# Optimization experiments

Measured on AMD Instinct MI355X. Metric: run time of the kernel, lower is better.

The kernel has to match this reference:

```python
import jax, jax.numpy as jnp
import numpy as np

B, L, HE, HD, E, AP, T = 128, 128, 1024, 1024, 512, 512, 64

def _lstm_cell(x, h, c, W_ih, W_hh, b_ih, b_hh):
    # torch LSTMCell: gates ordered i, f, g, o
    g = x @ W_ih + b_ih + h @ W_hh + b_hh
    i, f, gg, o = jnp.split(g, 4, axis=-1)
    c_new = jax.nn.sigmoid(f) * c + jax.nn.sigmoid(i) * jnp.tanh(gg)
    h_new = jax.nn.sigmoid(o) * jnp.tanh(c_new)
    return h_new, c_new

def setup_inputs() -> dict:
    key = jax.random.key(0)
    ks = jax.random.split(key, 24)
    def rn(k, shape, scale=0.02):
        return jax.random.normal(k, shape, dtype=jnp.float32) * scale
    inp = {
        "enc_hiddens": jax.random.normal(ks[0], (B, L, HE), dtype=jnp.float32),
        "enc_masks": jnp.zeros((B, L), dtype=jnp.int32),
        "h1_0": rn(ks[1], (B, HD), 1.0), "c1_0": rn(ks[2], (B, HD), 1.0),
        "h2_0": rn(ks[3], (B, HD), 1.0), "c2_0": rn(ks[4], (B, HD), 1.0),
        "captions": jax.random.normal(ks[5], (T, B, E), dtype=jnp.float32),
        # attention params
        "att_W": rn(ks[6], (HE, AP)), "att_b": jnp.zeros((AP,), jnp.float32),
        "dhp_W": rn(ks[7], (HD, AP)), "dhp_b": jnp.zeros((AP,), jnp.float32),
        "corr_w": rn(ks[8], (AP,)), "corr_b": jnp.zeros((), jnp.float32),
        "lt_W": rn(ks[9], (HD, HD)), "lt_b": jnp.zeros((HD,), jnp.float32),
        # LSTM cell 1: input E + HE
        "W_ih1": rn(ks[10], (E + HE, 4 * HD)), "W_hh1": rn(ks[11], (HD, 4 * HD)),
        "b_ih1": jnp.zeros((4 * HD,), jnp.float32), "b_hh1": jnp.zeros((4 * HD,), jnp.float32),
        # LSTM cell 2: input HD
        "W_ih2": rn(ks[12], (HD, 4 * HD)), "W_hh2": rn(ks[13], (HD, 4 * HD)),
        "b_ih2": jnp.zeros((4 * HD,), jnp.float32), "b_hh2": jnp.zeros((4 * HD,), jnp.float32),
    }
    return inp

def reference(enc_hiddens, enc_masks, h1_0, c1_0, h2_0, c2_0, captions,
              att_W, att_b, dhp_W, dhp_b, corr_w, corr_b, lt_W, lt_b,
              W_ih1, W_hh1, b_ih1, b_hh1, W_ih2, W_hh2, b_ih2, b_hh2):
    mask = enc_masks.astype(bool)                      # True == masked (pad)
    enc_proj = enc_hiddens @ att_W + att_b             # (B, L, AP)
    h_prev0 = jnp.ones((enc_hiddens.shape[0], HD), dtype=enc_hiddens.dtype) / HE

    def step(carry, x_t):
        h_prev, h1, c1, h2, c2 = carry
        q = h_prev @ dhp_W + dhp_b                     # (B, AP)
        e = jnp.tanh(enc_proj + q[:, None, :]) @ corr_w + corr_b  # (B, L)
        e = jnp.where(mask, -jnp.inf, e)
        alpha = jax.nn.softmax(e, axis=1)
        a_t = jnp.einsum('bl,blh->bh', alpha, enc_hiddens)
        lstm_in = jnp.concatenate([x_t, a_t], axis=1)
        h1n, c1n = _lstm_cell(lstm_in, h1, c1, W_ih1, W_hh1, b_ih1, b_hh1)
        h2n, c2n = _lstm_cell(h1n, h2, c2, W_ih2, W_hh2, b_ih2, b_hh2)
        # note: output uses layer-1 hidden (matches original); dropout is eval/no-op
        out_t = jnp.tanh(h1n @ lt_W + lt_b)
        # num_decoder_layers == 2 -> next h_prev is layer-2 hidden
        return (h2n, h1n, c1n, h2n, c2n), out_t

    _, outputs = jax.lax.scan(step, (h_prev0, h1_0, c1_0, h2_0, c2_0), captions)
    return outputs                                      # (T, B, HD)
```

## Files before the change

kernel.cpp:

```cpp
#include <hip/hip_runtime.h>
#include <cstdint>
#include <cstddef>

#define DEVI __device__ __forceinline__

typedef __attribute__((ext_vector_type(8))) short short8;
typedef __attribute__((ext_vector_type(4))) float floatx4;
typedef __attribute__((ext_vector_type(4))) unsigned short ushortx4;

DEVI float bf2f(unsigned short u) { union { unsigned int i; float f; } v; v.i = ((unsigned int)u) << 16; return v.f; }
DEVI unsigned short f2bf(float f) {
  union { float f; unsigned int i; } v; v.f = f;
  unsigned int r = v.i + 0x7fffu + ((v.i >> 16) & 1u);
  return (unsigned short)(r >> 16);
}
DEVI float fsig(float x) { return 1.f / (1.f + __expf(-x)); }
DEVI float ftanh(float x) { return 1.f - 2.f / (__expf(2.f * x) + 1.f); }

DEVI unsigned ld32s(const unsigned* p) { return __hip_atomic_load(p, __ATOMIC_RELAXED, __HIP_MEMORY_SCOPE_AGENT); }
DEVI void st32s(unsigned* p, unsigned v) { __hip_atomic_store(p, v, __ATOMIC_RELAXED, __HIP_MEMORY_SCOPE_AGENT); }
DEVI unsigned add32s(unsigned* p, unsigned v) { return __hip_atomic_fetch_add(p, v, __ATOMIC_RELAXED, __HIP_MEMORY_SCOPE_AGENT); }

DEVI void bar_nd() { asm volatile("s_waitcnt lgkmcnt(0)\ns_barrier" ::: "memory"); }

struct PP {
  const float *c1_0, *c2_0;
  const float *att_b, *dhp_b, *corr_w, *corr_b, *lt_b;
  const float *b_ih1, *b_hh1, *b_ih2, *b_hh2;
  const int* masks;
  float* out;
  unsigned int* SY; float* q0acc;
  const unsigned short* ench; unsigned short* proj; const unsigned short* caps;
  const unsigned short *W1t, *W2t, *dhpWt, *ltWt, *attWt;
  unsigned short* at; unsigned short* h1b; unsigned short* h2b; float* q;
  float *c1ws, *c2ws;
};

DEVI void zero_g(float* g) {
  for (int i = threadIdx.x; i < 128 * 17; i += 1024) g[i] = 0.f;
}

DEVI int swzb(int row, int kb) { return row * 256 + (kb ^ ((row & 7) << 4)); }

template <int NC, typename AL>
DEVI void gemm_lds(float* g, unsigned short (*As)[16384], unsigned short (*Bs)[2048],
                   const unsigned short* Wtile, int ldw, AL al) {
  const int tid = threadIdx.x, wave = tid >> 6, lane = tid & 63;
  const int sr = tid >> 4, sk8 = (tid & 15) << 3;
  const int wA0 = swzb(sr, (tid & 15) << 4);
  const int wA1 = swzb(sr + 64, (tid & 15) << 4);
  const int wB = swzb(sr & 15, (tid & 15) << 4);
  const unsigned short* wrow = Wtile + (size_t)sr * ldw;
  const int m = wave & 7, kh = wave >> 3;
  const int arow = (m << 4) + (lane & 15);
  const int kq = (lane >> 4) << 3;
  const int rA0 = swzb(arow, (kh * 64 + kq) << 1);
  const int rA1 = swzb(arow, (kh * 64 + 32 + kq) << 1);
  const int rB0 = swzb(lane & 15, (kh * 64 + kq) << 1);
  const int rB1 = swzb(lane & 15, (kh * 64 + 32 + kq) << 1);

  short8 aA[2], aB[2], bA, bB;
  floatx4 acc = (floatx4){0.f, 0.f, 0.f, 0.f};

#define LDCHUNK(c, ra, rb)                                        \
  do {                                                            \
    ra[0] = *(const short8*)al(sr, (c)*128 + sk8);                \
    ra[1] = *(const short8*)al(sr + 64, (c)*128 + sk8);           \
    if (tid < 256) rb = *(const short8*)(wrow + (c)*128 + sk8);   \
  } while (0)
#define STCHUNK(b, ra, rb)                                        \
  do {                                                            \
    char* ab_ = (char*)As[b];                                     \
    *(short8*)(ab_ + wA0) = ra[0];                                \
    *(short8*)(ab_ + wA1) = ra[1];                                \
    if (tid < 256) *(short8*)((char*)Bs[b] + wB) = rb;            \
  } while (0)
#define COMPCH(b)                                                 \
  do {                                                            \
    char* ab_ = (char*)As[b];                                     \
    char* bb_ = (char*)Bs[b];                                     \
    short8 x0 = *(const short8*)(ab_ + rA0);                      \
    short8 y0 = *(const short8*)(bb_ + rB0);                      \
    short8 x1 = *(const short8*)(ab_ + rA1);                      \
    short8 y1 = *(const short8*)(bb_ + rB1);                      \
    acc = __builtin_amdgcn_mfma_f32_16x16x32_bf16(x0, y0, acc, 0, 0, 0); \
    acc = __builtin_amdgcn_mfma_f32_16x16x32_bf16(x1, y1, acc, 0, 0, 0); \
  } while (0)

  LDCHUNK(0, aA, bA);
  LDCHUNK(1, aB, bB);
  STCHUNK(0, aA, bA);
  bar_nd();
#pragma unroll
  for (int c = 0; c < NC; c += 2) {
    if (c + 2 < NC) LDCHUNK(c + 2, aA, bA);
    COMPCH(0);
    STCHUNK(1, aB, bB);
    bar_nd();
    if (c + 3 < NC) LDCHUNK(c + 3, aB, bB);
    COMPCH(1);
    if (c + 2 < NC) STCHUNK(0, aA, bA);
    bar_nd();
  }
#undef LDCHUNK
#undef STCHUNK
#undef COMPCH

  const int col = lane & 15, rr = (lane >> 4) << 2;
#pragma unroll
  for (int r = 0; r < 4; ++r)
    atomicAdd(&g[((m << 4) + rr + r) * 17 + col], acc[r]);
}

DEVI int qidx(int a) { return a + (a >> 6); }

__global__ __launch_bounds__(1024, 4) void k1_attn(PP p, int t) {
  __shared__ float g[128 * 17];
  __shared__ unsigned short As[2][16384];
  __shared__ unsigned short Bs[2][2048];
  __shared__ float q_ss[520], corr_ss[520];
  __shared__ float alpha_s[128], e_s[128];
  __shared__ float redv[2];
  const int tid = threadIdx.x, blk = blockIdx.x;
  const int wave = tid >> 6, lane = tid & 63;

  if (blk < 32) {
    if (t >= 1 && t < 64) {
      zero_g(g);
      const unsigned short* h2p = p.h2b + ((((unsigned)t + 1u) & 1u) << 17);
      auto al = [&](int row, int k) -> const unsigned short* {
        return h2p + ((size_t)row << 10) + k;
      };
      gemm_lds<8>(g, As, Bs, p.dhpWt + (size_t)blk * 16 * 1024, 1024, al);
      __syncthreads();
      for (int e = tid; e < 2048; e += 1024) {
        const int b = e >> 4, col = e & 15, n = blk * 16 + col;
        const float qv = g[b * 17 + col] + p.dhp_b[n];
        st32s((unsigned*)(p.q + b * 512 + n), __float_as_uint(qv));
      }
      __builtin_amdgcn_s_waitcnt(0);
    }
    __syncthreads();
    if (tid == 0) add32s(&p.SY[4], 1u);
  } else if (blk < 160) {
    if (t < 64) {
      const int b = blk - 32;
      if (t >= 1) {
        if (tid == 0) {
          while (ld32s(&p.SY[4]) < (unsigned)(32 * (t + 1))) __builtin_amdgcn_s_sleep(1);
        }
        __syncthreads();
        if (tid < 512) q_ss[qidx(tid)] = __uint_as_float(ld32s((const unsigned*)(p.q + b * 512 + tid)));
      } else {
        if (tid < 512) q_ss[qidx(tid)] = p.q[b * 512 + tid];
      }
      if (tid < 512) corr_ss[qidx(tid)] = p.corr_w[tid];
      __syncthreads();
      {
        const int l = tid >> 3, l8 = tid & 7;
        const unsigned short* pp_ = p.proj + ((size_t)(b * 128 + l)) * 512 + l8 * 64;
        short8 vv[8];
#pragma unroll
        for (int j = 0; j < 8; ++j) vv[j] = *(const short8*)(pp_ + j * 8);
        float acc = 0.f;
#pragma unroll
        for (int j = 0; j < 8; ++j)
#pragma unroll
          for (int i = 0; i < 8; ++i) {
            const int ap = l8 * 64 + j * 8 + i;
            acc += ftanh(bf2f((unsigned short)vv[j][i]) + q_ss[qidx(ap)]) * corr_ss[qidx(ap)];
          }
        acc += __shfl_down(acc, 4, 8);
        acc += __shfl_down(acc, 2, 8);
        acc += __shfl_down(acc, 1, 8);
        if (l8 == 0) {
          acc += p.corr_b[0];
          if (p.masks[b * 128 + l] != 0) acc = -1e30f;
          e_s[l] = acc;
        }
      }
      __syncthreads();
      if (wave == 0) {
        float m0 = fmaxf(e_s[lane], e_s[lane + 64]);
#pragma unroll
        for (int off = 32; off; off >>= 1) m0 = fmaxf(m0, __shfl_xor(m0, off));
        const float a0 = __expf(e_s[lane] - m0), a1 = __expf(e_s[lane + 64] - m0);
        alpha_s[lane] = a0; alpha_s[lane + 64] = a1;
        float s = a0 + a1;
#pragma unroll
        for (int off = 32; off; off >>= 1) s += __shfl_xor(s, off);
        if (lane == 0) redv[0] = 1.f / s;
      }
      __syncthreads();
      {
        const float inv = redv[0];
        const unsigned short* pe = p.ench + ((size_t)b << 17) + tid;
        float acc = 0.f;
#pragma unroll 16
        for (int l = 0; l < 128; ++l) acc += alpha_s[l] * bf2f(pe[(size_t)l << 10]);
        p.at[(b << 10) + tid] = f2bf(acc * inv);
      }
    }
  } else {
    if (t >= 1) {
      const int ob = blk - 160, ot = t - 1;
      zero_g(g);
      const unsigned short* h1 = p.h1b + (((unsigned)ot & 1u) << 17);
      auto al = [&](int row, int k) -> const unsigned short* {
        return h1 + ((size_t)row << 10) + k;
      };
      gemm_lds<8>(g, As, Bs, p.ltWt + (size_t)ob * 16 * 1024, 1024, al);
      __syncthreads();
      for (int e = tid; e < 2048; e += 1024) {
        const int b = e >> 4, col = e & 15, n = ob * 16 + col;
        p.out[(size_t)ot * 131072 + (b << 10) + n] = ftanh(g[b * 17 + col] + p.lt_b[n]);
      }
    }
  }
}

__global__ __launch_bounds__(1024, 4) void k2_g1(PP p, int t) {
  __shared__ float g[128 * 17];
  __shared__ unsigned short As[2][16384];
  __shared__ unsigned short Bs[2][2048];
  const int tid = threadIdx.x, blk = blockIdx.x;
  zero_g(g);
  const unsigned short* caps_t = p.caps + ((size_t)t << 16);
  const unsigned short* h1p = p.h1b + ((((unsigned)t + 1u) & 1u) << 17);
  const unsigned short* at_ = p.at;
  auto al = [&](int row, int k) -> const unsigned short* {
    if (k < 512) return caps_t + ((size_t)row << 9) + k;
    if (k < 1536) return at_ + ((size_t)row << 10) + (k - 512);
    return h1p + ((size_t)row << 10) + (k - 1536);
  };
  gemm_lds<20>(g, As, Bs, p.W1t + (size_t)blk * 16 * 2560, 2560, al);
  __syncthreads();
  if (tid < 512) {
    const int b = tid >> 2, c = tid & 3;
    const int cidx = b * 1024 + blk * 4 + c;
    const float cprev = (t == 0) ? p.c1_0[cidx] : p.c1ws[cidx];
    const float gi = g[b * 17 + c]      + p.b_ih1[blk * 4 + c]        + p.b_hh1[blk * 4 + c];
    const float gf = g[b * 17 + 4 + c]  + p.b_ih1[1024 + blk * 4 + c] + p.b_hh1[1024 + blk * 4 + c];
    const float gg = g[b * 17 + 8 + c]  + p.b_ih1[2048 + blk * 4 + c] + p.b_hh1[2048 + blk * 4 + c];
    const float go = g[b * 17 + 12 + c] + p.b_ih1[3072 + blk * 4 + c] + p.b_hh1[3072 + blk * 4 + c];
    const float cn = fsig(gf) * cprev + fsig(gi) * ftanh(gg);
    p.c1ws[cidx] = cn;
    p.h1b[(((unsigned)t & 1u) << 17) + (b << 10) + blk * 4 + c] = f2bf(fsig(go) * ftanh(cn));
  }
}

__global__ __launch_bounds__(1024, 4) void k3_g2(PP p, int t) {
  __shared__ float g[128 * 17];
  __shared__ unsigned short As[2][16384];
  __shared__ unsigned short Bs[2][2048];
  const int tid = threadIdx.x, blk = blockIdx.x;
  zero_g(g);
  const unsigned short* h1c = p.h1b + (((unsigned)t & 1u) << 17);
  const unsigned short* h2p = p.h2b + ((((unsigned)t + 1u) & 1u) << 17);
  auto al = [&](int row, int k) -> const unsigned short* {
    if (k < 1024) return h1c + ((size_t)row << 10) + k;
    return h2p + ((size_t)row << 10) + (k - 1024);
  };
  gemm_lds<16>(g, As, Bs, p.W2t + (size_t)blk * 16 * 2048, 2048, al);
  __syncthreads();
  if (tid < 512) {
    const int b = tid >> 2, c = tid & 3;
    const int cidx = b * 1024 + blk * 4 + c;
    const float cprev = (t == 0) ? p.c2_0[cidx] : p.c2ws[cidx];
    const float gi = g[b * 17 + c]      + p.b_ih2[blk * 4 + c]        + p.b_hh2[blk * 4 + c];
    const float gf = g[b * 17 + 4 + c]  + p.b_ih2[1024 + blk * 4 + c] + p.b_hh2[1024 + blk * 4 + c];
    const float gg = g[b * 17 + 8 + c]  + p.b_ih2[2048 + blk * 4 + c] + p.b_hh2[2048 + blk * 4 + c];
    const float go = g[b * 17 + 12 + c] + p.b_ih2[3072 + blk * 4 + c] + p.b_hh2[3072 + blk * 4 + c];
    const float cn = fsig(gf) * cprev + fsig(gi) * ftanh(gg);
    p.c2ws[cidx] = cn;
    p.h2b[(((unsigned)t & 1u) << 17) + (b << 10) + blk * 4 + c] = f2bf(fsig(go) * ftanh(cn));
  }
}

__global__ __launch_bounds__(512) void k_zero(unsigned int* SY, float* q0) {
  SY[threadIdx.x] = 0u;
  q0[threadIdx.x] = 0.f;
}

__global__ __launch_bounds__(256) void k_cvt4(const float* caps, const float* ench,
                                              const float* h1_0, const float* h2_0,
                                              unsigned short* o_caps, unsigned short* o_ench,
                                              unsigned short* o_h1, unsigned short* o_h2) {
  const size_t i = ((size_t)blockIdx.x * 256 + threadIdx.x) << 2;
  const float* s; unsigned short* d; size_t off;
  if (i < 4194304u) { s = caps; d = o_caps; off = i; }
  else if (i < 20971520u) { s = ench; d = o_ench; off = i - 4194304u; }
  else if (i < 21102592u) { s = h1_0; d = o_h1; off = i - 20971520u; }
  else { s = h2_0; d = o_h2; off = i - 21102592u; }
  floatx4 v = *(const floatx4*)(s + off);
  ushortx4 o = { f2bf(v[0]), f2bf(v[1]), f2bf(v[2]), f2bf(v[3]) };
  *(ushortx4*)(d + off) = o;
}

__global__ __launch_bounds__(256) void k_tr(const float* srcA, const float* srcB, int ksplit,
                                            int K, int stride, int Nrows, int perm,
                                            unsigned short* out, float* q0) {
  __shared__ float lds[64][5];
  const int nbr = Nrows >> 2;
  const int rt = blockIdx.x % nbr, kt = blockIdx.x / nbr;
  const int r0 = rt * 4, k0 = kt * 64;
  int oc0;
  if (perm) { const int nb = r0 >> 4, gg = (r0 & 15) >> 2; oc0 = gg * 1024 + nb * 4; }
  else oc0 = r0;
  {
    const int kk = threadIdx.x >> 2, rr = threadIdx.x & 3;
    const int k = k0 + kk;
    const float* s = (k < ksplit) ? (srcA + (size_t)k * stride) : (srcB + (size_t)(k - ksplit) * stride);
    lds[kk][rr] = s[oc0 + rr];
  }
  __syncthreads();
  if (q0 != nullptr && threadIdx.x < 4) {
    float t = 0.f;
    for (int kk = 0; kk < 64; ++kk) t += lds[kk][threadIdx.x];
    atomicAdd(&q0[oc0 + threadIdx.x], t);
  }
  {
    const int rr = threadIdx.x >> 6, kk = threadIdx.x & 63;
    out[(size_t)(r0 + rr) * K + k0 + kk] = f2bf(lds[kk][rr]);
  }
}

__global__ __launch_bounds__(1024, 4) void k_proj2(PP p) {
  __shared__ unsigned short As[2][16384];
  __shared__ unsigned short Bs[2][16384];
  const int tid = threadIdx.x, blk = blockIdx.x;
  const int mb = blk >> 2, nb = blk & 3;
  const int m0 = mb << 7, n0 = nb << 7;
  const int wave = tid >> 6, lane = tid & 63;
  const int sr = tid >> 4, sk8 = (tid & 15) << 3;
  const int wL0 = swzb(sr, (tid & 15) << 4);
  const int wL1 = swzb(sr + 64, (tid & 15) << 4);
  const int mw = wave & 7, nh = wave >> 3;
  const int m16 = lane & 15, kq = (lane >> 4) << 3;
  const unsigned short* Ag  = p.ench  + ((size_t)(m0 + sr) << 10);
  const unsigned short* Ag2 = p.ench  + ((size_t)(m0 + sr + 64) << 10);
  const unsigned short* Bg  = p.attWt + ((size_t)(n0 + sr) << 10);
  const unsigned short* Bg2 = p.attWt + ((size_t)(n0 + sr + 64) << 10);

  const int ar = mw * 16 + m16;
  const int aBase = ar * 256, aX = (ar & 7) << 4;
  const int bX = (m16 & 7) << 4;
  int bBase[4];
#pragma unroll
  for (int nf = 0; nf < 4; ++nf) bBase[nf] = (nh * 64 + nf * 16 + m16) * 256;

  floatx4 acc[4];
#pragma unroll
  for (int nf = 0; nf < 4; ++nf) acc[nf] = (floatx4){0.f, 0.f, 0.f, 0.f};

  short8 xa0, xa1, xb0, xb1, ya0, ya1, yb0, yb1;

#define PJLD(c, r0_, r1_, r2_, r3_)                      \
  do {                                                   \
    r0_ = *(const short8*)(Ag + (c) * 128 + sk8);        \
    r1_ = *(const short8*)(Ag2 + (c) * 128 + sk8);       \
    r2_ = *(const short8*)(Bg + (c) * 128 + sk8);        \
    r3_ = *(const short8*)(Bg2 + (c) * 128 + sk8);       \
  } while (0)
#define PJST(b, r0_, r1_, r2_, r3_)                      \
  do {                                                   \
    *(short8*)((char*)As[b] + wL0) = r0_;                \
    *(short8*)((char*)As[b] + wL1) = r1_;                \
    *(short8*)((char*)Bs[b] + wL0) = r2_;                \
    *(short8*)((char*)Bs[b] + wL1) = r3_;                \
  } while (0)
#define PJCOMP(b)                                                        \
  do {                                                                   \
    char* ab_ = (char*)As[b];                                            \
    char* bb_ = (char*)Bs[b];                                            \
    _Pragma("unroll")                                                    \
    for (int ks = 0; ks < 4; ++ks) {                                     \
      const int kb = ks * 64 + (kq << 1);                                \
      short8 af = *(const short8*)(ab_ + aBase + (kb ^ aX));             \
      _Pragma("unroll")                                                  \
      for (int nf = 0; nf < 4; ++nf) {                                   \
        short8 bf = *(const short8*)(bb_ + bBase[nf] + (kb ^ bX));       \
        acc[nf] = __builtin_amdgcn_mfma_f32_16x16x32_bf16(af, bf, acc[nf], 0, 0, 0); \
      }                                                                  \
    }                                                                    \
  } while (0)

  PJLD(0, xa0, xa1, xb0, xb1);
  PJLD(1, ya0, ya1, yb0, yb1);
  PJST(0, xa0, xa1, xb0, xb1);
  bar_nd();
#pragma unroll
  for (int c = 0; c < 8; c += 2) {
    if (c + 2 < 8) PJLD(c + 2, xa0, xa1, xb0, xb1);
    PJCOMP(0);
    PJST(1, ya0, ya1, yb0, yb1);
    bar_nd();
    if (c + 3 < 8) PJLD(c + 3, ya0, ya1, yb0, yb1);
    PJCOMP(1);
    if (c + 2 < 8) PJST(0, xa0, xa1, xb0, xb1);
    bar_nd();
  }
#undef PJLD
#undef PJST
#undef PJCOMP

  const int r0 = (lane >> 4) << 2;
#pragma unroll
  for (int nf = 0; nf < 4; ++nf) {
    const int col = n0 + nh * 64 + nf * 16 + m16;
    const float ab = p.att_b[col];
#pragma unroll
    for (int r = 0; r < 4; ++r) {
      const int row = m0 + mw * 16 + r0 + r;
      p.proj[(size_t)row * 512 + col] = f2bf(acc[nf][r] + ab);
    }
  }
}

__global__ __launch_bounds__(1024) void k_qinit(float* q, const float* q0acc, const float* dhp_b) {
  const int i = blockIdx.x * 1024 + threadIdx.x;
  const int n = i & 511;
  q[i] = q0acc[n] * (1.f / 1024.f) + dhp_b[n];
}

extern "C" void kernel_launch(void* const* d_in, const int* in_sizes, int n_in,
                              void* d_out, int out_size, void* d_ws, size_t ws_size,
                              hipStream_t stream) {
  const float* enc_hiddens = (const float*)d_in[0];
  const int*   enc_masks   = (const int*)d_in[1];
  const float* h1_0 = (const float*)d_in[2];
  const float* c1_0 = (const float*)d_in[3];
  const float* h2_0 = (const float*)d_in[4];
  const float* c2_0 = (const float*)d_in[5];
  const float* captions = (const float*)d_in[6];
  const float* att_W = (const float*)d_in[7];
  const float* att_b = (const float*)d_in[8];
  const float* dhp_W = (const float*)d_in[9];
  const float* dhp_b = (const float*)d_in[10];
  const float* corr_w = (const float*)d_in[11];
  const float* corr_b = (const float*)d_in[12];
  const float* lt_W = (const float*)d_in[13];
  const float* lt_b = (const float*)d_in[14];
  const float* W_ih1 = (const float*)d_in[15];
  const float* W_hh1 = (const float*)d_in[16];
  const float* b_ih1 = (const float*)d_in[17];
  const float* b_hh1 = (const float*)d_in[18];
  const float* W_ih2 = (const float*)d_in[19];
  const float* W_hh2 = (const float*)d_in[20];
  const float* b_ih2 = (const float*)d_in[21];
  const float* b_hh2 = (const float*)d_in[22];

  uint8_t* w = (uint8_t*)d_ws;
  unsigned int* SY = (unsigned int*)w;
  float* q0acc = (float*)(w + 2048);
  size_t off = 4096;
  unsigned short* ench  = (unsigned short*)(w + off); off += 33554432;
  unsigned short* proj  = (unsigned short*)(w + off); off += 16777216;
  unsigned short* caps  = (unsigned short*)(w + off); off += 8388608;
  unsigned short* W1t   = (unsigned short*)(w + off); off += 20971520;
  unsigned short* W2t   = (unsigned short*)(w + off); off += 16777216;
  unsigned short* dhpWt = (unsigned short*)(w + off); off += 1048576;
  unsigned short* ltWt  = (unsigned short*)(w + off); off += 2097152;
  unsigned short* attWt = (unsigned short*)(w + off); off += 1048576;
  unsigned short* at_   = (unsigned short*)(w + off); off += 262144;
  unsigned short* h1b   = (unsigned short*)(w + off); off += 524288;
  unsigned short* h2b   = (unsigned short*)(w + off); off += 524288;
  float* qb             = (float*)(w + off);          off += 262144;
  float* c1ws           = (float*)(w + off);          off += 524288;
  float* c2ws           = (float*)(w + off);          off += 524288;
  if (ws_size < off) return;

  k_zero<<<1, 512, 0, stream>>>(SY, q0acc);
  k_cvt4<<<20736, 256, 0, stream>>>(captions, enc_hiddens, h1_0, h2_0,
                                    caps, ench, h1b + 131072, h2b + 131072);
  k_tr<<<40960, 256, 0, stream>>>(W_ih1, W_hh1, 1536, 2560, 4096, 4096, 1, W1t, nullptr);
  k_tr<<<32768, 256, 0, stream>>>(W_ih2, W_hh2, 1024, 2048, 4096, 4096, 1, W2t, nullptr);
  k_tr<<<2048, 256, 0, stream>>>(dhp_W, dhp_W, 1024, 1024, 512, 512, 0, dhpWt, q0acc);
  k_tr<<<4096, 256, 0, stream>>>(lt_W, lt_W, 1024, 1024, 1024, 1024, 0, ltWt, nullptr);
  k_tr<<<2048, 256, 0, stream>>>(att_W, att_W, 1024, 1024, 512, 512, 0, attWt, nullptr);
  k_qinit<<<64, 1024, 0, stream>>>(qb, q0acc, dhp_b);

  PP p;
  p.c1_0 = c1_0; p.c2_0 = c2_0;
  p.att_b = att_b; p.dhp_b = dhp_b; p.corr_w = corr_w; p.corr_b = corr_b; p.lt_b = lt_b;
  p.b_ih1 = b_ih1; p.b_hh1 = b_hh1; p.b_ih2 = b_ih2; p.b_hh2 = b_hh2;
  p.masks = enc_masks;
  p.out = (float*)d_out;
  p.SY = SY; p.q0acc = q0acc;
  p.ench = ench; p.proj = proj; p.caps = caps;
  p.W1t = W1t; p.W2t = W2t; p.dhpWt = dhpWt; p.ltWt = ltWt; p.attWt = attWt;
  p.at = at_; p.h1b = h1b; p.h2b = h2b; p.q = qb;
  p.c1ws = c1ws; p.c2ws = c2ws;

  k_proj2<<<512, 1024, 0, stream>>>(p);

  for (int t = 0; t < 64; ++t) {
    k1_attn<<<224, 1024, 0, stream>>>(p, t);
    k2_g1<<<256, 1024, 0, stream>>>(p, t);
    k3_g2<<<256, 1024, 0, stream>>>(p, t);
  }
  k1_attn<<<224, 1024, 0, stream>>>(p, 64);
}
```

Measured before the change: 4.831 ms.

## Fuse per-step kernels into one persistent kernel with global flag barriers

```diff
diff --git a/kernel.cpp b/kernel.cpp
--- a/kernel.cpp
+++ b/kernel.cpp
@@ -19,7 +19,18 @@
 
 DEVI unsigned ld32s(const unsigned* p) { return __hip_atomic_load(p, __ATOMIC_RELAXED, __HIP_MEMORY_SCOPE_AGENT); }
 DEVI void st32s(unsigned* p, unsigned v) { __hip_atomic_store(p, v, __ATOMIC_RELAXED, __HIP_MEMORY_SCOPE_AGENT); }
-DEVI unsigned add32s(unsigned* p, unsigned v) { return __hip_atomic_fetch_add(p, v, __ATOMIC_RELAXED, __HIP_MEMORY_SCOPE_AGENT); }
+
+DEVI void wait_ge(unsigned* f, unsigned tgt) {
+  if (threadIdx.x == 0) {
+    while (ld32s(f) < tgt) __builtin_amdgcn_s_sleep(1);
+    (void)__hip_atomic_load(f, __ATOMIC_ACQUIRE, __HIP_MEMORY_SCOPE_AGENT);
+  }
+  __syncthreads();
+}
+DEVI void sig1(unsigned* f) {
+  if (threadIdx.x == 0)
+    (void)__hip_atomic_fetch_add(f, 1u, __ATOMIC_RELEASE, __HIP_MEMORY_SCOPE_AGENT);
+}
 
 DEVI void bar_nd() { asm volatile("s_waitcnt lgkmcnt(0)\ns_barrier" ::: "memory"); }
 
@@ -114,7 +125,7 @@
 
 DEVI int qidx(int a) { return a + (a >> 6); }
 
-__global__ __launch_bounds__(1024, 4) void k1_attn(PP p, int t) {
+__global__ __launch_bounds__(1024, 4) void k_all(PP p) {
   __shared__ float g[128 * 17];
   __shared__ unsigned short As[2][16384];
   __shared__ unsigned short Bs[2][2048];
@@ -123,38 +134,39 @@
   __shared__ float redv[2];
   const int tid = threadIdx.x, blk = blockIdx.x;
   const int wave = tid >> 6, lane = tid & 63;
-
-  if (blk < 32) {
-    if (t >= 1 && t < 64) {
-      zero_g(g);
-      const unsigned short* h2p = p.h2b + ((((unsigned)t + 1u) & 1u) << 17);
-      auto al = [&](int row, int k) -> const unsigned short* {
-        return h2p + ((size_t)row << 10) + k;
-      };
-      gemm_lds<8>(g, As, Bs, p.dhpWt + (size_t)blk * 16 * 1024, 1024, al);
-      __syncthreads();
-      for (int e = tid; e < 2048; e += 1024) {
-        const int b = e >> 4, col = e & 15, n = blk * 16 + col;
-        const float qv = g[b * 17 + col] + p.dhp_b[n];
-        st32s((unsigned*)(p.q + b * 512 + n), __float_as_uint(qv));
-      }
-      __builtin_amdgcn_s_waitcnt(0);
-    }
-    __syncthreads();
-    if (tid == 0) add32s(&p.SY[4], 1u);
-  } else if (blk < 160) {
-    if (t < 64) {
+  unsigned* F = p.SY;
+
+  if (blk >= 32 && blk < 160) {
+    if (tid < 512) corr_ss[qidx(tid)] = p.corr_w[tid];
+  }
+
+  for (int t = 0; t < 64; ++t) {
+    if (blk < 32) {
+      if (t >= 1) {
+        wait_ge(&F[4 * (t - 1) + 3], 256);
+        zero_g(g);
+        const unsigned short* h2p = p.h2b + ((((unsigned)t + 1u) & 1u) << 17);
+        auto al = [&](int row, int k) -> const unsigned short* {
+          return h2p + ((size_t)row << 10) + k;
+        };
+        gemm_lds<8>(g, As, Bs, p.dhpWt + (size_t)blk * 16 * 1024, 1024, al);
+        __syncthreads();
+        for (int e = tid; e < 2048; e += 1024) {
+          const int b = e >> 4, col = e & 15, n = blk * 16 + col;
+          st32s((unsigned*)(p.q + b * 512 + n), __float_as_uint(g[b * 17 + col] + p.dhp_b[n]));
+        }
+        __builtin_amdgcn_s_waitcnt(0);
+        __syncthreads();
+        sig1(&F[4 * t + 0]);
+      }
+    } else if (blk < 160) {
       const int b = blk - 32;
       if (t >= 1) {
-        if (tid == 0) {
-          while (ld32s(&p.SY[4]) < (unsigned)(32 * (t + 1))) __builtin_amdgcn_s_sleep(1);
-        }
-        __syncthreads();
+        wait_ge(&F[4 * t + 0], 32);
         if (tid < 512) q_ss[qidx(tid)] = __uint_as_float(ld32s((const unsigned*)(p.q + b * 512 + tid)));
       } else {
         if (tid < 512) q_ss[qidx(tid)] = p.q[b * 512 + tid];
       }
-      if (tid < 512) corr_ss[qidx(tid)] = p.corr_w[tid];
       __syncthreads();
       {
         const int l = tid >> 3, l8 = tid & 7;
@@ -200,80 +212,95 @@
         for (int l = 0; l < 128; ++l) acc += alpha_s[l] * bf2f(pe[(size_t)l << 10]);
         p.at[(b << 10) + tid] = f2bf(acc * inv);
       }
+      __builtin_amdgcn_s_waitcnt(0);
+      __syncthreads();
+      sig1(&F[4 * t + 1]);
+    } else if (blk < 224) {
+      if (t >= 1) {
+        const int ob = blk - 160, ot = t - 1;
+        zero_g(g);
+        const unsigned short* h1 = p.h1b + (((unsigned)ot & 1u) << 17);
+        auto al = [&](int row, int k) -> const unsigned short* {
+          return h1 + ((size_t)row << 10) + k;
+        };
+        gemm_lds<8>(g, As, Bs, p.ltWt + (size_t)ob * 16 * 1024, 1024, al);
+        __syncthreads();
+        for (int e = tid; e < 2048; e += 1024) {
+          const int b = e >> 4, col = e & 15, n = ob * 16 + col;
+          p.out[(size_t)ot * 131072 + (b << 10) + n] = ftanh(g[b * 17 + col] + p.lt_b[n]);
+        }
+      }
     }
-  } else {
-    if (t >= 1) {
-      const int ob = blk - 160, ot = t - 1;
-      zero_g(g);
-      const unsigned short* h1 = p.h1b + (((unsigned)ot & 1u) << 17);
+    wait_ge(&F[4 * t + 1], 128);
+    zero_g(g);
+    {
+      const unsigned short* caps_t = p.caps + ((size_t)t << 16);
+      const unsigned short* h1p = p.h1b + ((((unsigned)t + 1u) & 1u) << 17);
+      const unsigned short* at_ = p.at;
       auto al = [&](int row, int k) -> const unsigned short* {
-        return h1 + ((size_t)row << 10) + k;
+        if (k < 512) return caps_t + ((size_t)row << 9) + k;
+        if (k < 1536) return at_ + ((size_t)row << 10) + (k - 512);
+        return h1p + ((size_t)row << 10) + (k - 1536);
       };
-      gemm_lds<8>(g, As, Bs, p.ltWt + (size_t)ob * 16 * 1024, 1024, al);
+      gemm_lds<20>(g, As, Bs, p.W1t + (size_t)blk * 16 * 2560, 2560, al);
       __syncthreads();
-      for (int e = tid; e < 2048; e += 1024) {
-        const int b = e >> 4, col = e & 15, n = ob * 16 + col;
-        p.out[(size_t)ot * 131072 + (b << 10) + n] = ftanh(g[b * 17 + col] + p.lt_b[n]);
+      if (tid < 512) {
+        const int b = tid >> 2, c = tid & 3;
+        const int cidx = b * 1024 + blk * 4 + c;
+        const float cprev = (t == 0) ? p.c1_0[cidx] : p.c1ws[cidx];
+        const float gi = g[b * 17 + c]      + p.b_ih1[blk * 4 + c]        + p.b_hh1[blk * 4 + c];
+        const float gf = g[b * 17 + 4 + c]  + p.b_ih1[1024 + blk * 4 + c] + p.b_hh1[1024 + blk * 4 + c];
+        const float gg = g[b * 17 + 8 + c]  + p.b_ih1[2048 + blk * 4 + c] + p.b_hh1[2048 + blk * 4 + c];
+        const float go = g[b * 17 + 12 + c] + p.b_ih1[3072 + blk * 4 + c] + p.b_hh1[3072 + blk * 4 + c];
+        const float cn = fsig(gf) * cprev + fsig(gi) * ftanh(gg);
+        p.c1ws[cidx] = cn;
+        p.h1b[(((unsigned)t & 1u) << 17) + (b << 10) + blk * 4 + c] = f2bf(fsig(go) * ftanh(cn));
       }
     }
-  }
-}
-
-__global__ __launch_bounds__(1024, 4) void k2_g1(PP p, int t) {
-  __shared__ float g[128 * 17];
-  __shared__ unsigned short As[2][16384];
-  __shared__ unsigned short Bs[2][2048];
-  const int tid = threadIdx.x, blk = blockIdx.x;
-  zero_g(g);
-  const unsigned short* caps_t = p.caps + ((size_t)t << 16);
-  const unsigned short* h1p = p.h1b + ((((unsigned)t + 1u) & 1u) << 17);
-  const unsigned short* at_ = p.at;
-  auto al = [&](int row, int k) -> const unsigned short* {
-    if (k < 512) return caps_t + ((size_t)row << 9) + k;
-    if (k < 1536) return at_ + ((size_t)row << 10) + (k - 512);
-    return h1p + ((size_t)row << 10) + (k - 1536);
-  };
-  gemm_lds<20>(g, As, Bs, p.W1t + (size_t)blk * 16 * 2560, 2560, al);
-  __syncthreads();
-  if (tid < 512) {
-    const int b = tid >> 2, c = tid & 3;
-    const int cidx = b * 1024 + blk * 4 + c;
-    const float cprev = (t == 0) ? p.c1_0[cidx] : p.c1ws[cidx];
-    const float gi = g[b * 17 + c]      + p.b_ih1[blk * 4 + c]        + p.b_hh1[blk * 4 + c];
-    const float gf = g[b * 17 + 4 + c]  + p.b_ih1[1024 + blk * 4 + c] + p.b_hh1[1024 + blk * 4 + c];
-    const float gg = g[b * 17 + 8 + c]  + p.b_ih1[2048 + blk * 4 + c] + p.b_hh1[2048 + blk * 4 + c];
-    const float go = g[b * 17 + 12 + c] + p.b_ih1[3072 + blk * 4 + c] + p.b_hh1[3072 + blk * 4 + c];
-    const float cn = fsig(gf) * cprev + fsig(gi) * ftanh(gg);
-    p.c1ws[cidx] = cn;
-    p.h1b[(((unsigned)t & 1u) << 17) + (b << 10) + blk * 4 + c] = f2bf(fsig(go) * ftanh(cn));
-  }
-}
-
-__global__ __launch_bounds__(1024, 4) void k3_g2(PP p, int t) {
-  __shared__ float g[128 * 17];
-  __shared__ unsigned short As[2][16384];
-  __shared__ unsigned short Bs[2][2048];
-  const int tid = threadIdx.x, blk = blockIdx.x;
-  zero_g(g);
-  const unsigned short* h1c = p.h1b + (((unsigned)t & 1u) << 17);
-  const unsigned short* h2p = p.h2b + ((((unsigned)t + 1u) & 1u) << 17);
-  auto al = [&](int row, int k) -> const unsigned short* {
-    if (k < 1024) return h1c + ((size_t)row << 10) + k;
-    return h2p + ((size_t)row << 10) + (k - 1024);
-  };
-  gemm_lds<16>(g, As, Bs, p.W2t + (size_t)blk * 16 * 2048, 2048, al);
-  __syncthreads();
-  if (tid < 512) {
-    const int b = tid >> 2, c = tid & 3;
-    const int cidx = b * 1024 + blk * 4 + c;
-    const float cprev = (t == 0) ? p.c2_0[cidx] : p.c2ws[cidx];
-    const float gi = g[b * 17 + c]      + p.b_ih2[blk * 4 + c]        + p.b_hh2[blk * 4 + c];
-    const float gf = g[b * 17 + 4 + c]  + p.b_ih2[1024 + blk * 4 + c] + p.b_hh2[1024 + blk * 4 + c];
-    const float gg = g[b * 17 + 8 + c]  + p.b_ih2[2048 + blk * 4 + c] + p.b_hh2[2048 + blk * 4 + c];
-    const float go = g[b * 17 + 12 + c] + p.b_ih2[3072 + blk * 4 + c] + p.b_hh2[3072 + blk * 4 + c];
-    const float cn = fsig(gf) * cprev + fsig(gi) * ftanh(gg);
-    p.c2ws[cidx] = cn;
-    p.h2b[(((unsigned)t & 1u) << 17) + (b << 10) + blk * 4 + c] = f2bf(fsig(go) * ftanh(cn));
+    __builtin_amdgcn_s_waitcnt(0);
+    __syncthreads();
+    sig1(&F[4 * t + 2]);
+    wait_ge(&F[4 * t + 2], 256);
+    zero_g(g);
+    {
+      const unsigned short* h1c = p.h1b + (((unsigned)t & 1u) << 17);
+      const unsigned short* h2p = p.h2b + ((((unsigned)t + 1u) & 1u) << 17);
+      auto al = [&](int row, int k) -> const unsigned short* {
+        if (k < 1024) return h1c + ((size_t)row << 10) + k;
+        return h2p + ((size_t)row << 10) + (k - 1024);
+      };
+      gemm_lds<16>(g, As, Bs, p.W2t + (size_t)blk * 16 * 2048, 2048, al);
+      __syncthreads();
+      if (tid < 512) {
+        const int b = tid >> 2, c = tid & 3;
+        const int cidx = b * 1024 + blk * 4 + c;
+        const float cprev = (t == 0) ? p.c2_0[cidx] : p.c2ws[cidx];
+        const float gi = g[b * 17 + c]      + p.b_ih2[blk * 4 + c]        + p.b_hh2[blk * 4 + c];
+        const float gf = g[b * 17 + 4 + c]  + p.b_ih2[1024 + blk * 4 + c] + p.b_hh2[1024 + blk * 4 + c];
+        const float gg = g[b * 17 + 8 + c]  + p.b_ih2[2048 + blk * 4 + c] + p.b_hh2[2048 + blk * 4 + c];
+        const float go = g[b * 17 + 12 + c] + p.b_ih2[3072 + blk * 4 + c] + p.b_hh2[3072 + blk * 4 + c];
+        const float cn = fsig(gf) * cprev + fsig(gi) * ftanh(gg);
+        p.c2ws[cidx] = cn;
+        p.h2b[(((unsigned)t & 1u) << 17) + (b << 10) + blk * 4 + c] = f2bf(fsig(go) * ftanh(cn));
+      }
+    }
+    __builtin_amdgcn_s_waitcnt(0);
+    __syncthreads();
+    sig1(&F[4 * t + 3]);
+  }
+  if (blk >= 160 && blk < 224) {
+    const int ob = blk - 160;
+    zero_g(g);
+    const unsigned short* h1 = p.h1b + (1u << 17);
+    auto al = [&](int row, int k) -> const unsigned short* {
+      return h1 + ((size_t)row << 10) + k;
+    };
+    gemm_lds<8>(g, As, Bs, p.ltWt + (size_t)ob * 16 * 1024, 1024, al);
+    __syncthreads();
+    for (int e = tid; e < 2048; e += 1024) {
+      const int b = e >> 4, col = e & 15, n = ob * 16 + col;
+      p.out[(size_t)63 * 131072 + (b << 10) + n] = ftanh(g[b * 17 + col] + p.lt_b[n]);
+    }
   }
 }
 
@@ -493,11 +520,5 @@
   p.c1ws = c1ws; p.c2ws = c2ws;
 
   k_proj2<<<512, 1024, 0, stream>>>(p);
-
-  for (int t = 0; t < 64; ++t) {
-    k1_attn<<<224, 1024, 0, stream>>>(p, t);
-    k2_g1<<<256, 1024, 0, stream>>>(p, t);
-    k3_g2<<<256, 1024, 0, stream>>>(p, t);
-  }
-  k1_attn<<<224, 1024, 0, stream>>>(p, 64);
-}
+  k_all<<<256, 1024, 0, stream>>>(p);
+}
```

Measured after the change: 9.496 ms. 1.97x slower.

## Fuse LSTM layer kernels with atomic counter sync and per-step history buffers

Applied to the files above, without the earlier changes.

```diff
diff --git a/kernel.cpp b/kernel.cpp
--- a/kernel.cpp
+++ b/kernel.cpp
@@ -127,7 +127,7 @@
   if (blk < 32) {
     if (t >= 1 && t < 64) {
       zero_g(g);
-      const unsigned short* h2p = p.h2b + ((((unsigned)t + 1u) & 1u) << 17);
+      const unsigned short* h2p = p.h2b + (size_t)(t - 1) * 131072;
       auto al = [&](int row, int k) -> const unsigned short* {
         return h2p + ((size_t)row << 10) + k;
       };
@@ -135,8 +135,7 @@
       __syncthreads();
       for (int e = tid; e < 2048; e += 1024) {
         const int b = e >> 4, col = e & 15, n = blk * 16 + col;
-        const float qv = g[b * 17 + col] + p.dhp_b[n];
-        st32s((unsigned*)(p.q + b * 512 + n), __float_as_uint(qv));
+        st32s((unsigned*)(p.q + b * 512 + n), __float_as_uint(g[b * 17 + col] + p.dhp_b[n]));
       }
       __builtin_amdgcn_s_waitcnt(0);
     }
@@ -145,6 +144,12 @@
   } else if (blk < 160) {
     if (t < 64) {
       const int b = blk - 32;
+      const int l = tid >> 3, l8 = tid & 7;
+      const unsigned short* pp_ = p.proj + ((size_t)(b * 128 + l)) * 512 + l8 * 64;
+      short8 vv[8];
+#pragma unroll
+      for (int j = 0; j < 8; ++j) vv[j] = *(const short8*)(pp_ + j * 8);
+      if (tid < 512) corr_ss[qidx(tid)] = p.corr_w[tid];
       if (t >= 1) {
         if (tid == 0) {
           while (ld32s(&p.SY[4]) < (unsigned)(32 * (t + 1))) __builtin_amdgcn_s_sleep(1);
@@ -154,14 +159,8 @@
       } else {
         if (tid < 512) q_ss[qidx(tid)] = p.q[b * 512 + tid];
       }
-      if (tid < 512) corr_ss[qidx(tid)] = p.corr_w[tid];
       __syncthreads();
       {
-        const int l = tid >> 3, l8 = tid & 7;
-        const unsigned short* pp_ = p.proj + ((size_t)(b * 128 + l)) * 512 + l8 * 64;
-        short8 vv[8];
-#pragma unroll
-        for (int j = 0; j < 8; ++j) vv[j] = *(const short8*)(pp_ + j * 8);
         float acc = 0.f;
 #pragma unroll
         for (int j = 0; j < 8; ++j)
@@ -197,15 +196,15 @@
         const unsigned short* pe = p.ench + ((size_t)b << 17) + tid;
         float acc = 0.f;
 #pragma unroll 16
-        for (int l = 0; l < 128; ++l) acc += alpha_s[l] * bf2f(pe[(size_t)l << 10]);
-        p.at[(b << 10) + tid] = f2bf(acc * inv);
+        for (int l2 = 0; l2 < 128; ++l2) acc += alpha_s[l2] * bf2f(pe[(size_t)l2 << 10]);
+        p.at[(size_t)t * 131072 + (b << 10) + tid] = f2bf(acc * inv);
       }
     }
   } else {
     if (t >= 1) {
       const int ob = blk - 160, ot = t - 1;
       zero_g(g);
-      const unsigned short* h1 = p.h1b + (((unsigned)ot & 1u) << 17);
+      const unsigned short* h1 = p.h1b + (size_t)ot * 131072;
       auto al = [&](int row, int k) -> const unsigned short* {
         return h1 + ((size_t)row << 10) + k;
       };
@@ -219,21 +218,29 @@
   }
 }
 
-__global__ __launch_bounds__(1024, 4) void k2_g1(PP p, int t) {
+__global__ __launch_bounds__(1024, 4) void k23(PP p, int t) {
   __shared__ float g[128 * 17];
   __shared__ unsigned short As[2][16384];
   __shared__ unsigned short Bs[2][2048];
   const int tid = threadIdx.x, blk = blockIdx.x;
+  unsigned* Ch1 = p.SY + 64;
+  const unsigned short* caps_t = p.caps + ((size_t)t << 16);
+  const unsigned short* atcur = p.at + (size_t)t * 131072;
+  const int prev = (t == 0) ? 64 : t - 1;
+  const unsigned short* h1prev = p.h1b + (size_t)prev * 131072;
+  const unsigned short* h2prev = p.h2b + (size_t)prev * 131072;
+  unsigned short* h1cur = p.h1b + (size_t)t * 131072;
+  unsigned short* h2cur = p.h2b + (size_t)t * 131072;
+
   zero_g(g);
-  const unsigned short* caps_t = p.caps + ((size_t)t << 16);
-  const unsigned short* h1p = p.h1b + ((((unsigned)t + 1u) & 1u) << 17);
-  const unsigned short* at_ = p.at;
-  auto al = [&](int row, int k) -> const unsigned short* {
-    if (k < 512) return caps_t + ((size_t)row << 9) + k;
-    if (k < 1536) return at_ + ((size_t)row << 10) + (k - 512);
-    return h1p + ((size_t)row << 10) + (k - 1536);
-  };
-  gemm_lds<20>(g, As, Bs, p.W1t + (size_t)blk * 16 * 2560, 2560, al);
+  {
+    auto al = [&](int row, int k) -> const unsigned short* {
+      if (k < 512) return caps_t + ((size_t)row << 9) + k;
+      if (k < 1536) return atcur + ((size_t)row << 10) + (k - 512);
+      return h1prev + ((size_t)row << 10) + (k - 1536);
+    };
+    gemm_lds<20>(g, As, Bs, p.W1t + (size_t)blk * 16 * 2560, 2560, al);
+  }
   __syncthreads();
   if (tid < 512) {
     const int b = tid >> 2, c = tid & 3;
@@ -245,23 +252,36 @@
     const float go = g[b * 17 + 12 + c] + p.b_ih1[3072 + blk * 4 + c] + p.b_hh1[3072 + blk * 4 + c];
     const float cn = fsig(gf) * cprev + fsig(gi) * ftanh(gg);
     p.c1ws[cidx] = cn;
-    p.h1b[(((unsigned)t & 1u) << 17) + (b << 10) + blk * 4 + c] = f2bf(fsig(go) * ftanh(cn));
-  }
-}
-
-__global__ __launch_bounds__(1024, 4) void k3_g2(PP p, int t) {
-  __shared__ float g[128 * 17];
-  __shared__ unsigned short As[2][16384];
-  __shared__ unsigned short Bs[2][2048];
-  const int tid = threadIdx.x, blk = blockIdx.x;
+    unsigned hv = (unsigned)f2bf(fsig(go) * ftanh(cn));
+    unsigned pv = __shfl_down(hv, 1);
+    if (!(tid & 1)) st32s((unsigned*)(h1cur + (b << 10) + blk * 4 + c), hv | (pv << 16));
+  }
+  __builtin_amdgcn_s_waitcnt(0);
+  __syncthreads();
+  if (tid == 0) add32s(&Ch1[4 * t + (blk & 3)], 1u);
+
   zero_g(g);
-  const unsigned short* h1c = p.h1b + (((unsigned)t & 1u) << 17);
-  const unsigned short* h2p = p.h2b + ((((unsigned)t + 1u) & 1u) << 17);
-  auto al = [&](int row, int k) -> const unsigned short* {
-    if (k < 1024) return h1c + ((size_t)row << 10) + k;
-    return h2p + ((size_t)row << 10) + (k - 1024);
-  };
-  gemm_lds<16>(g, As, Bs, p.W2t + (size_t)blk * 16 * 2048, 2048, al);
+  {
+    auto al = [&](int row, int k) -> const unsigned short* {
+      return h2prev + ((size_t)row << 10) + k;
+    };
+    gemm_lds<8>(g, As, Bs, p.W2t + (size_t)blk * 16 * 2048 + 1024, 2048, al);
+  }
+  if (tid == 0) {
+    unsigned* c4 = &Ch1[4 * t];
+    for (;;) {
+      unsigned s = ld32s(&c4[0]) + ld32s(&c4[1]) + ld32s(&c4[2]) + ld32s(&c4[3]);
+      if (s >= 256u) break;
+      __builtin_amdgcn_s_sleep(4);
+    }
+  }
+  __syncthreads();
+  {
+    auto al = [&](int row, int k) -> const unsigned short* {
+      return h1cur + ((size_t)row << 10) + k;
+    };
+    gemm_lds<8>(g, As, Bs, p.W2t + (size_t)blk * 16 * 2048, 2048, al);
+  }
   __syncthreads();
   if (tid < 512) {
     const int b = tid >> 2, c = tid & 3;
@@ -273,13 +293,13 @@
     const float go = g[b * 17 + 12 + c] + p.b_ih2[3072 + blk * 4 + c] + p.b_hh2[3072 + blk * 4 + c];
     const float cn = fsig(gf) * cprev + fsig(gi) * ftanh(gg);
     p.c2ws[cidx] = cn;
-    p.h2b[(((unsigned)t & 1u) << 17) + (b << 10) + blk * 4 + c] = f2bf(fsig(go) * ftanh(cn));
-  }
-}
-
-__global__ __launch_bounds__(512) void k_zero(unsigned int* SY, float* q0) {
+    h2cur[(b << 10) + blk * 4 + c] = f2bf(fsig(go) * ftanh(cn));
+  }
+}
+
+__global__ __launch_bounds__(1024) void k_zero(unsigned int* SY, float* q0) {
   SY[threadIdx.x] = 0u;
-  q0[threadIdx.x] = 0.f;
+  if (threadIdx.x < 512) q0[threadIdx.x] = 0.f;
 }
 
 __global__ __launch_bounds__(256) void k_cvt4(const float* caps, const float* ench,
@@ -452,8 +472,8 @@
 
   uint8_t* w = (uint8_t*)d_ws;
   unsigned int* SY = (unsigned int*)w;
-  float* q0acc = (float*)(w + 2048);
-  size_t off = 4096;
+  float* q0acc = (float*)(w + 4096);
+  size_t off = 8192;
   unsigned short* ench  = (unsigned short*)(w + off); off += 33554432;
   unsigned short* proj  = (unsigned short*)(w + off); off += 16777216;
   unsigned short* caps  = (unsigned short*)(w + off); off += 8388608;
@@ -462,17 +482,18 @@
   unsigned short* dhpWt = (unsigned short*)(w + off); off += 1048576;
   unsigned short* ltWt  = (unsigned short*)(w + off); off += 2097152;
   unsigned short* attWt = (unsigned short*)(w + off); off += 1048576;
-  unsigned short* at_   = (unsigned short*)(w + off); off += 262144;
-  unsigned short* h1b   = (unsigned short*)(w + off); off += 524288;
-  unsigned short* h2b   = (unsigned short*)(w + off); off += 524288;
+  unsigned short* at_   = (unsigned short*)(w + off); off += 16777216;
+  unsigned short* h1b   = (unsigned short*)(w + off); off += 17039360;
+  unsigned short* h2b   = (unsigned short*)(w + off); off += 17039360;
   float* qb             = (float*)(w + off);          off += 262144;
   float* c1ws           = (float*)(w + off);          off += 524288;
   float* c2ws           = (float*)(w + off);          off += 524288;
   if (ws_size < off) return;
 
-  k_zero<<<1, 512, 0, stream>>>(SY, q0acc);
+  k_zero<<<1, 1024, 0, stream>>>(SY, q0acc);
   k_cvt4<<<20736, 256, 0, stream>>>(captions, enc_hiddens, h1_0, h2_0,
-                                    caps, ench, h1b + 131072, h2b + 131072);
+                                    caps, ench,
+                                    h1b + (size_t)64 * 131072, h2b + (size_t)64 * 131072);
   k_tr<<<40960, 256, 0, stream>>>(W_ih1, W_hh1, 1536, 2560, 4096, 4096, 1, W1t, nullptr);
   k_tr<<<32768, 256, 0, stream>>>(W_ih2, W_hh2, 1024, 2048, 4096, 4096, 1, W2t, nullptr);
   k_tr<<<2048, 256, 0, stream>>>(dhp_W, dhp_W, 1024, 1024, 512, 512, 0, dhpWt, q0acc);
@@ -496,8 +517,7 @@
 
   for (int t = 0; t < 64; ++t) {
     k1_attn<<<224, 1024, 0, stream>>>(p, t);
-    k2_g1<<<256, 1024, 0, stream>>>(p, t);
-    k3_g2<<<256, 1024, 0, stream>>>(p, t);
+    k23<<<256, 1024, 0, stream>>>(p, t);
   }
   k1_attn<<<224, 1024, 0, stream>>>(p, 64);
 }
```

After: 5.064 ms. +4.8%, slower.
